# Optimization experiments

Measured on AMD Instinct MI355X. Metric: run time of the kernel, lower is better.

## Reference

```python
import jax, jax.numpy as jnp
import numpy as np

N = 8192
F_IN, F1, F2 = 11, 16, 32
HEADS = 3
D_CAT = 2 * F2          # 64, concat of interface + neighborhood branches
D_POOL = D_CAT * HEADS  # 192


def setup_inputs() -> dict:
    key = jax.random.key(0)
    ks = jax.random.split(key, 16)
    s = 0.1
    return {
        "x_int": jax.random.normal(ks[0], (N, F_IN), jnp.float32),
        "x_nh": jax.random.normal(ks[1], (N, F_IN), jnp.float32),
        # dense soft adjacencies, scaled ~1/N so aggregates stay O(1)
        "adj_int": jax.random.uniform(ks[2], (N, N), jnp.float32) / N,
        "adj_nh": jax.random.uniform(ks[3], (N, N), jnp.float32) / N,
        "W1_int": jax.random.normal(ks[4], (F_IN, F1), jnp.float32) * s,
        "b1_int": jnp.zeros((F1,), jnp.float32),
        "W1_nh": jax.random.normal(ks[5], (F_IN, F1), jnp.float32) * s,
        "b1_nh": jnp.zeros((F1,), jnp.float32),
        "W2_int": jax.random.normal(ks[6], (F1, F2), jnp.float32) * s,
        "b2_int": jnp.zeros((F2,), jnp.float32),
        "W2_nh": jax.random.normal(ks[7], (F1, F2), jnp.float32) * s,
        "b2_nh": jnp.zeros((F2,), jnp.float32),
        "W_att": jax.random.normal(ks[8], (D_CAT, HEADS), jnp.float32) * s,
        "W_dense": jax.random.normal(ks[9], (D_POOL, 1), jnp.float32) * s,
        "b_dense": jnp.zeros((1,), jnp.float32),
    }


def _dgcn(A, x, W, b):
    # diffusion graph conv: aggregate neighbors then linear + relu
    return jax.nn.relu(A @ (x @ W) + b)


def reference(x_int, x_nh, adj_int, adj_nh,
              W1_int, b1_int, W1_nh, b1_nh,
              W2_int, b2_int, W2_nh, b2_nh,
              W_att, W_dense, b_dense):
    # conv1 / conv2, two parallel graph branches
    h_int = _dgcn(adj_int, x_int, W1_int, b1_int)   # [N, 16]
    h_nh = _dgcn(adj_nh, x_nh, W1_nh, b1_nh)        # [N, 16]
    h_int = _dgcn(adj_int, h_int, W2_int, b2_int)   # [N, 32]
    h_nh = _dgcn(adj_nh, h_nh, W2_nh, b2_nh)        # [N, 32]
    h = jnp.concatenate([h_int, h_nh], axis=1)      # [N, 64]
    # multi-head tanh self-attention pooling over nodes
    scores = jnp.tanh(h @ W_att)                    # [N, heads]
    att = jax.nn.softmax(scores, axis=0)            # softmax over nodes
    pooled = jnp.einsum('nh,nd->hd', att, h).reshape(1, D_POOL)  # [1, 192]
    out = pooled @ W_dense + b_dense                # [1, 1]
    return jnp.squeeze(out, 1)                      # [1]
```

## Files before the change

kernel.cpp:

```cpp
#include <hip/hip_runtime.h>


constexpr int N = 8192;

__global__ void k_dense_in(const float* __restrict__ x0, const float* __restrict__ x1,
                           const float* __restrict__ W0, const float* __restrict__ W1,
                           float* __restrict__ o0, float* __restrict__ o1) {
    const int branch = blockIdx.y;
    const float* __restrict__ x = branch ? x1 : x0;
    const float* __restrict__ W = branch ? W1 : W0;
    float* __restrict__ o = branch ? o1 : o0;
    __shared__ float sW[11 * 16];
    if (threadIdx.x < 176) sW[threadIdx.x] = W[threadIdx.x];
    __syncthreads();
    const int n = blockIdx.x * blockDim.x + threadIdx.x;
    float xr[11];
#pragma unroll
    for (int j = 0; j < 11; ++j) xr[j] = x[n * 11 + j];
    float acc[16];
#pragma unroll
    for (int f = 0; f < 16; ++f) acc[f] = 0.f;
#pragma unroll
    for (int j = 0; j < 11; ++j)
#pragma unroll
        for (int f = 0; f < 16; ++f) acc[f] += xr[j] * sW[j * 16 + f];
#pragma unroll
    for (int f = 0; f < 16; ++f) o[f * N + n] = acc[f];
}

__global__ void k_dense_mid(const float* __restrict__ h0, const float* __restrict__ h1,
                            const float* __restrict__ W0, const float* __restrict__ W1,
                            float* __restrict__ o0, float* __restrict__ o1) {
    const int branch = blockIdx.y;
    const float* __restrict__ h = branch ? h1 : h0;
    const float* __restrict__ W = branch ? W1 : W0;
    float* __restrict__ o = branch ? o1 : o0;
    __shared__ float sW[16 * 32];
    for (int i = threadIdx.x; i < 512; i += blockDim.x) sW[i] = W[i];
    __syncthreads();
    const int n = blockIdx.x * blockDim.x + threadIdx.x;
    float hr[16];
#pragma unroll
    for (int q = 0; q < 4; ++q)
        *reinterpret_cast<float4*>(&hr[q * 4]) =
            *reinterpret_cast<const float4*>(&h[n * 16 + q * 4]);
    float acc[32];
#pragma unroll
    for (int f = 0; f < 32; ++f) acc[f] = 0.f;
#pragma unroll
    for (int j = 0; j < 16; ++j)
#pragma unroll
        for (int f = 0; f < 32; ++f) acc[f] += hr[j] * sW[j * 32 + f];
#pragma unroll
    for (int f = 0; f < 32; ++f) o[f * N + n] = acc[f];
}

template <int F>
__global__ __launch_bounds__(256, F == 16 ? 3 : 2) void k_spmm(
    const float* __restrict__ A0, const float* __restrict__ A1,
    const float* __restrict__ PT0, const float* __restrict__ PT1,
    const float* __restrict__ b0, const float* __restrict__ b1,
    float* __restrict__ o0, float* __restrict__ o1, int ostride) {
    constexpr int Fw = F / 4;
    constexpr int M = 8;
    constexpr int KT = 256;
    constexpr int NT = N / KT;
    constexpr int NV = M * Fw;
    const int branch = blockIdx.y;
    const float* __restrict__ A = branch ? A1 : A0;
    const float* __restrict__ PT = branch ? PT1 : PT0;
    const float* __restrict__ bias = branch ? b1 : b0;
    float* __restrict__ o = branch ? o1 : o0;

    const int lane = threadIdx.x & 63;
    const int wave = threadIdx.x >> 6;
    const int f0 = wave * Fw;
    const int r0 = blockIdx.x * M;
    const int phase = blockIdx.x & (NT - 1);

    const float* __restrict__ Abase = A + (size_t)r0 * N + 4 * lane;
    const float* __restrict__ Pbase = PT + (size_t)f0 * N + 4 * lane;

    float4 a[M], an[M], pt[Fw];
    float acc[M][Fw];
#pragma unroll
    for (int m = 0; m < M; ++m)
#pragma unroll
        for (int j = 0; j < Fw; ++j) acc[m][j] = 0.f;

    auto K0of = [&](int t) { return ((t + phase) & (NT - 1)) * KT; };
    auto loadA = [&](float4(&buf)[M], int K0) {
#pragma unroll
        for (int m = 0; m < M; ++m)
            buf[m] = *reinterpret_cast<const float4*>(Abase + (size_t)m * N + K0);
    };
    auto loadP = [&](int K0) {
#pragma unroll
        for (int j = 0; j < Fw; ++j)
            pt[j] = *reinterpret_cast<const float4*>(Pbase + (size_t)j * N + K0);
    };
    auto fmas = [&](float4(&buf)[M]) {
#pragma unroll
        for (int m = 0; m < M; ++m)
#pragma unroll
            for (int j = 0; j < Fw; ++j) {
                acc[m][j] += buf[m].x * pt[j].x;
                acc[m][j] += buf[m].y * pt[j].y;
                acc[m][j] += buf[m].z * pt[j].z;
                acc[m][j] += buf[m].w * pt[j].w;
            }
    };

    loadA(a, K0of(0));
    for (int t = 0; t < NT; t += 2) {
        loadP(K0of(t));
        loadA(an, K0of(t + 1));
        __builtin_amdgcn_s_barrier();
        fmas(a);
        loadP(K0of(t + 1));
        if (t + 2 < NT) loadA(a, K0of(t + 2));
        __builtin_amdgcn_s_barrier();
        fmas(an);
    }

    float v[NV];
#pragma unroll
    for (int i = 0; i < NV; ++i) v[i] = acc[i / Fw][i % Fw];
#pragma unroll
    for (int s = 0; (NV >> s) > 1; ++s) {
        const int bit = (lane >> s) & 1;
#pragma unroll
        for (int i = 0; i < (NV >> s); i += 2) {
            const float t0 = __shfl_xor(v[i], 1 << s);
            const float t1 = __shfl_xor(v[i + 1], 1 << s);
            v[i >> 1] = bit ? (v[i + 1] + t1) : (v[i] + t0);
        }
    }
    float r = v[0];
    if constexpr (NV == 32) r += __shfl_xor(r, 32);

    const int m = lane / Fw;
    const int j = lane % Fw;
    if (F == 32 || lane < 32) {
        const float val = fmaxf(r + bias[f0 + j], 0.f);
        o[(size_t)(r0 + m) * ostride + f0 + j] = val;
    }
}

__global__ void k_att_pool(const float* __restrict__ h, const float* __restrict__ Watt,
                           const float* __restrict__ Wd, float* __restrict__ partials) {
    __shared__ float sWa[64 * 3];
    __shared__ float sWd[192];
    for (int i = threadIdx.x; i < 192; i += blockDim.x) {
        sWa[i] = Watt[i];
        sWd[i] = Wd[i];
    }
    __syncthreads();
    const int n = blockIdx.x * blockDim.x + threadIdx.x;
    float hv[64];
#pragma unroll
    for (int q = 0; q < 16; ++q)
        *reinterpret_cast<float4*>(&hv[q * 4]) =
            *reinterpret_cast<const float4*>(&h[(size_t)n * 64 + q * 4]);
    float s0 = 0.f, s1 = 0.f, s2 = 0.f;
#pragma unroll
    for (int d = 0; d < 64; ++d) {
        s0 += hv[d] * sWa[d * 3 + 0];
        s1 += hv[d] * sWa[d * 3 + 1];
        s2 += hv[d] * sWa[d * 3 + 2];
    }
    float dot0 = 0.f, dot1 = 0.f, dot2 = 0.f;
#pragma unroll
    for (int d = 0; d < 64; ++d) {
        dot0 += hv[d] * sWd[0 * 64 + d];
        dot1 += hv[d] * sWd[1 * 64 + d];
        dot2 += hv[d] * sWd[2 * 64 + d];
    }
    const float e0 = expf(tanhf(s0));
    const float e1 = expf(tanhf(s1));
    const float e2 = expf(tanhf(s2));
    float vals[6] = {e0, e1, e2, e0 * dot0, e1 * dot1, e2 * dot2};
#pragma unroll
    for (int i = 0; i < 6; ++i) {
        float v = vals[i];
#pragma unroll
        for (int off = 1; off < 64; off <<= 1) v += __shfl_xor(v, off);
        vals[i] = v;
    }
    __shared__ float sred[4][6];
    const int wave = threadIdx.x >> 6, lane = threadIdx.x & 63;
    if (lane == 0) {
#pragma unroll
        for (int i = 0; i < 6; ++i) sred[wave][i] = vals[i];
    }
    __syncthreads();
    if (threadIdx.x == 0) {
#pragma unroll
        for (int i = 0; i < 6; ++i)
            partials[blockIdx.x * 6 + i] = sred[0][i] + sred[1][i] + sred[2][i] + sred[3][i];
    }
}

__global__ void k_att_final(const float* __restrict__ partials, const float* __restrict__ bd,
                            float* __restrict__ out) {
    if (threadIdx.x == 0) {
        float Z0 = 0.f, Z1 = 0.f, Z2 = 0.f, U0 = 0.f, U1 = 0.f, U2 = 0.f;
        for (int b = 0; b < 32; ++b) {
            Z0 += partials[b * 6 + 0];
            Z1 += partials[b * 6 + 1];
            Z2 += partials[b * 6 + 2];
            U0 += partials[b * 6 + 3];
            U1 += partials[b * 6 + 4];
            U2 += partials[b * 6 + 5];
        }
        out[0] = U0 / Z0 + U1 / Z1 + U2 / Z2 + bd[0];
    }
}

extern "C" void kernel_launch(void* const* d_in, const int* in_sizes, int n_in,
                              void* d_out, int out_size, void* d_ws, size_t ws_size,
                              hipStream_t stream) {
    const float* x_int   = (const float*)d_in[0];
    const float* x_nh    = (const float*)d_in[1];
    const float* adj_int = (const float*)d_in[2];
    const float* adj_nh  = (const float*)d_in[3];
    const float* W1_int  = (const float*)d_in[4];
    const float* b1_int  = (const float*)d_in[5];
    const float* W1_nh   = (const float*)d_in[6];
    const float* b1_nh   = (const float*)d_in[7];
    const float* W2_int  = (const float*)d_in[8];
    const float* b2_int  = (const float*)d_in[9];
    const float* W2_nh   = (const float*)d_in[10];
    const float* b2_nh   = (const float*)d_in[11];
    const float* W_att   = (const float*)d_in[12];
    const float* W_dense = (const float*)d_in[13];
    const float* b_dense = (const float*)d_in[14];

    float* ws = (float*)d_ws;
    float* P1T_0 = ws;
    float* P1T_1 = ws + 131072;
    float* H1_0  = ws + 262144;
    float* H1_1  = ws + 393216;
    float* P2T_0 = ws + 524288;
    float* P2T_1 = ws + 786432;
    float* hcat  = ws + 1048576;
    float* partials = ws + 1572864;
    float* out = (float*)d_out;

    k_dense_in<<<dim3(32, 2), 256, 0, stream>>>(x_int, x_nh, W1_int, W1_nh, P1T_0, P1T_1);
    k_spmm<16><<<dim3(1024, 2), 256, 0, stream>>>(adj_int, adj_nh, P1T_0, P1T_1,
                                                  b1_int, b1_nh, H1_0, H1_1, 16);
    k_dense_mid<<<dim3(32, 2), 256, 0, stream>>>(H1_0, H1_1, W2_int, W2_nh, P2T_0, P2T_1);
    k_spmm<32><<<dim3(1024, 2), 256, 0, stream>>>(adj_int, adj_nh, P2T_0, P2T_1,
                                                  b2_int, b2_nh, hcat, hcat + 32, 64);
    k_att_pool<<<32, 256, 0, stream>>>(hcat, W_att, W_dense, partials);
    k_att_final<<<1, 64, 0, stream>>>(partials, b_dense, out);
}
```

Before: 626.5 us.

## Split-K dense SpMM with LDS-staged P tiles and separate reduction kernel

Restructures the adjacency-times-features kernels into a split-K scheme. Each 512-thread block handles 128 rows and one K slice, stages the transposed P slice into shared memory in two feature halves, and streams A rows with double buffering. Partial sums go to a workspace and are combined by a new reduce kernel that adds bias and applies ReLU. The aim is to cut redundant global reads of P and raise reuse and occupancy in the memory-bound A stream. The cost is an extra partials write and read plus an additional kernel launch per layer.

After: 1.565 ms. 2.5x slower.

```diff
diff --git a/kernel.cpp b/kernel.cpp
--- a/kernel.cpp
+++ b/kernel.cpp
@@ -1,4 +1,5 @@
 #include <hip/hip_runtime.h>
+#include <type_traits>
 
 
 constexpr int N = 8192;
@@ -56,95 +57,151 @@
 }
 
 template <int F>
-__global__ __launch_bounds__(256, F == 16 ? 3 : 2) void k_spmm(
+__global__ __launch_bounds__(512, 2) void k_spmm(
     const float* __restrict__ A0, const float* __restrict__ A1,
     const float* __restrict__ PT0, const float* __restrict__ PT1,
-    const float* __restrict__ b0, const float* __restrict__ b1,
-    float* __restrict__ o0, float* __restrict__ o1, int ostride) {
-    constexpr int Fw = F / 4;
-    constexpr int M = 8;
-    constexpr int KT = 256;
-    constexpr int NT = N / KT;
-    constexpr int NV = M * Fw;
-    const int branch = blockIdx.y;
-    const float* __restrict__ A = branch ? A1 : A0;
-    const float* __restrict__ PT = branch ? PT1 : PT0;
-    const float* __restrict__ bias = branch ? b1 : b0;
-    float* __restrict__ o = branch ? o1 : o0;
-
-    const int lane = threadIdx.x & 63;
-    const int wave = threadIdx.x >> 6;
-    const int f0 = wave * Fw;
-    const int r0 = blockIdx.x * M;
-    const int phase = blockIdx.x & (NT - 1);
-
-    const float* __restrict__ Abase = A + (size_t)r0 * N + 4 * lane;
-    const float* __restrict__ Pbase = PT + (size_t)f0 * N + 4 * lane;
-
-    float4 a[M], an[M], pt[Fw];
-    float acc[M][Fw];
-#pragma unroll
-    for (int m = 0; m < M; ++m)
-#pragma unroll
-        for (int j = 0; j < Fw; ++j) acc[m][j] = 0.f;
-
-    auto K0of = [&](int t) { return ((t + phase) & (NT - 1)) * KT; };
-    auto loadA = [&](float4(&buf)[M], int K0) {
-#pragma unroll
-        for (int m = 0; m < M; ++m)
-            buf[m] = *reinterpret_cast<const float4*>(Abase + (size_t)m * N + K0);
+    float* __restrict__ part) {
+    constexpr int W = 32768 / F;
+    constexpr int NS = N / W;
+    constexpr int C = W / 256;
+    constexpr int G2 = F / 8;
+    constexpr int NG = 8;
+    constexpr int RPB = 128;
+
+    const int br = blockIdx.y;
+    const float* __restrict__ A = br ? A1 : A0;
+    const float* __restrict__ PT = br ? PT1 : PT0;
+    float* __restrict__ pb = part + (size_t)br * NS * N * F;
+
+    __shared__ float plds[16384];
+
+    const int tid = threadIdx.x;
+    const int lane = tid & 63;
+    const int wave = tid >> 6;
+    const int rb = blockIdx.x / NS, sl = blockIdx.x % NS;
+    const int K0 = sl * W;
+    const int wrow0 = rb * RPB + wave * (2 * NG);
+
+    const float* __restrict__ Ab = A + (size_t)wrow0 * N + K0 + 4 * lane;
+
+    auto stage = [&](int half) {
+        const float* __restrict__ Ps = PT + (size_t)half * (F / 2) * N + K0;
+        for (int idx = tid; idx < (F / 2) * W; idx += 512) {
+            const int kk = idx & (W - 1);
+            const int fl = idx / W;
+            plds[((kk & 3) * G2 + (fl >> 2)) * W + ((kk >> 2) << 2) + (fl & 3)] =
+                Ps[(size_t)fl * N + kk];
+        }
     };
-    auto loadP = [&](int K0) {
-#pragma unroll
-        for (int j = 0; j < Fw; ++j)
-            pt[j] = *reinterpret_cast<const float4*>(Pbase + (size_t)j * N + K0);
+
+    float acc[2][F];
+#pragma unroll
+    for (int rr = 0; rr < 2; ++rr)
+#pragma unroll
+        for (int f = 0; f < F; ++f) acc[rr][f] = 0.f;
+
+    float4 Abuf[2][C], Bbuf[2][C];
+
+    auto ld = [&](float4(&buf)[2][C], int g) {
+#pragma unroll
+        for (int rr = 0; rr < 2; ++rr)
+#pragma unroll
+            for (int c = 0; c < C; ++c)
+                buf[rr][c] = *reinterpret_cast<const float4*>(
+                    Ab + (size_t)(2 * g + rr) * N + c * 256);
     };
-    auto fmas = [&](float4(&buf)[M]) {
-#pragma unroll
-        for (int m = 0; m < M; ++m)
-#pragma unroll
-            for (int j = 0; j < Fw; ++j) {
-                acc[m][j] += buf[m].x * pt[j].x;
-                acc[m][j] += buf[m].y * pt[j].y;
-                acc[m][j] += buf[m].z * pt[j].z;
-                acc[m][j] += buf[m].w * pt[j].w;
+
+    auto cmp = [&](auto Hc, float4(&buf)[2][C]) {
+        constexpr int HALF = decltype(Hc)::value;
+#pragma unroll
+        for (int c = 0; c < C; ++c)
+#pragma unroll
+            for (int t = 0; t < 4; ++t)
+#pragma unroll
+                for (int g = 0; g < G2; ++g) {
+                    const float4 pv = *reinterpret_cast<const float4*>(
+                        &plds[(t * G2 + g) * W + (c * 64 + lane) * 4]);
+#pragma unroll
+                    for (int rr = 0; rr < 2; ++rr) {
+                        const float av = (t == 0)   ? buf[rr][c].x
+                                         : (t == 1) ? buf[rr][c].y
+                                         : (t == 2) ? buf[rr][c].z
+                                                    : buf[rr][c].w;
+                        acc[rr][HALF * (F / 2) + g * 4 + 0] += av * pv.x;
+                        acc[rr][HALF * (F / 2) + g * 4 + 1] += av * pv.y;
+                        acc[rr][HALF * (F / 2) + g * 4 + 2] += av * pv.z;
+                        acc[rr][HALF * (F / 2) + g * 4 + 3] += av * pv.w;
+                    }
+                }
+    };
+
+    auto redstore = [&](int g) {
+        constexpr int NV = 2 * F;
+        float v[NV];
+#pragma unroll
+        for (int i = 0; i < NV; ++i) v[i] = acc[i / F][i % F];
+#pragma unroll
+        for (int s = 0; (NV >> s) > 1; ++s) {
+            const int bit = (lane >> s) & 1;
+#pragma unroll
+            for (int i = 0; i < (NV >> s); i += 2) {
+                const float t0 = __shfl_xor(v[i], 1 << s);
+                const float t1 = __shfl_xor(v[i + 1], 1 << s);
+                v[i >> 1] = bit ? (v[i + 1] + t1) : (v[i] + t0);
             }
+        }
+        float r = v[0];
+        if constexpr (NV == 32) {
+            r += __shfl_xor(r, 32);
+            if (lane < 32)
+                pb[((size_t)sl * N + wrow0 + 2 * g + (lane >> 4)) * F + (lane & 15)] = r;
+        } else {
+            pb[((size_t)sl * N + wrow0 + 2 * g + (lane >> 5)) * F + (lane & 31)] = r;
+        }
+#pragma unroll
+        for (int rr = 0; rr < 2; ++rr)
+#pragma unroll
+            for (int f = 0; f < F; ++f) acc[rr][f] = 0.f;
     };
 
-    loadA(a, K0of(0));
-    for (int t = 0; t < NT; t += 2) {
-        loadP(K0of(t));
-        loadA(an, K0of(t + 1));
-        __builtin_amdgcn_s_barrier();
-        fmas(a);
-        loadP(K0of(t + 1));
-        if (t + 2 < NT) loadA(a, K0of(t + 2));
-        __builtin_amdgcn_s_barrier();
-        fmas(an);
-    }
-
-    float v[NV];
-#pragma unroll
-    for (int i = 0; i < NV; ++i) v[i] = acc[i / Fw][i % Fw];
-#pragma unroll
-    for (int s = 0; (NV >> s) > 1; ++s) {
-        const int bit = (lane >> s) & 1;
-#pragma unroll
-        for (int i = 0; i < (NV >> s); i += 2) {
-            const float t0 = __shfl_xor(v[i], 1 << s);
-            const float t1 = __shfl_xor(v[i + 1], 1 << s);
-            v[i >> 1] = bit ? (v[i + 1] + t1) : (v[i] + t0);
-        }
-    }
-    float r = v[0];
-    if constexpr (NV == 32) r += __shfl_xor(r, 32);
-
-    const int m = lane / Fw;
-    const int j = lane % Fw;
-    if (F == 32 || lane < 32) {
-        const float val = fmaxf(r + bias[f0 + j], 0.f);
-        o[(size_t)(r0 + m) * ostride + f0 + j] = val;
-    }
+    using IC0 = std::integral_constant<int, 0>;
+    using IC1 = std::integral_constant<int, 1>;
+
+    stage(0);
+    ld(Abuf, 0);
+    __syncthreads();
+    for (int gp = 0; gp < NG; gp += 2) {
+        ld(Bbuf, gp + 1);
+        cmp(IC0{}, Abuf);
+        __syncthreads();
+        stage(1);
+        __syncthreads();
+        cmp(IC1{}, Abuf);
+        redstore(gp);
+        if (gp + 2 < NG) ld(Abuf, gp + 2);
+        cmp(IC1{}, Bbuf);
+        __syncthreads();
+        stage(0);
+        __syncthreads();
+        cmp(IC0{}, Bbuf);
+        redstore(gp + 1);
+    }
+}
+
+template <int F, int NS>
+__global__ void k_reduce(const float* __restrict__ part,
+                         const float* __restrict__ bias0, const float* __restrict__ bias1,
+                         float* __restrict__ o0, float* __restrict__ o1, int ostride) {
+    const int br = blockIdx.y;
+    const float* __restrict__ pb = part + (size_t)br * NS * N * F;
+    const float* __restrict__ bias = br ? bias1 : bias0;
+    float* __restrict__ o = br ? o1 : o0;
+    const int i = blockIdx.x * 256 + threadIdx.x;
+    const int r = i / F, f = i % F;
+    float s = bias[f];
+#pragma unroll
+    for (int sl = 0; sl < NS; ++sl) s += pb[(size_t)sl * N * F + i];
+    o[(size_t)r * ostride + f] = fmaxf(s, 0.f);
 }
 
 __global__ void k_att_pool(const float* __restrict__ h, const float* __restrict__ Watt,
@@ -244,15 +301,16 @@
     float* P2T_0 = ws + 524288;
     float* P2T_1 = ws + 786432;
     float* hcat  = ws + 1048576;
-    float* partials = ws + 1572864;
+    float* attp  = ws + 1572864;
+    float* part  = ws + 1573120;
     float* out = (float*)d_out;
 
     k_dense_in<<<dim3(32, 2), 256, 0, stream>>>(x_int, x_nh, W1_int, W1_nh, P1T_0, P1T_1);
-    k_spmm<16><<<dim3(1024, 2), 256, 0, stream>>>(adj_int, adj_nh, P1T_0, P1T_1,
-                                                  b1_int, b1_nh, H1_0, H1_1, 16);
+    k_spmm<16><<<dim3(256, 2), 512, 0, stream>>>(adj_int, adj_nh, P1T_0, P1T_1, part);
+    k_reduce<16, 4><<<dim3(512, 2), 256, 0, stream>>>(part, b1_int, b1_nh, H1_0, H1_1, 16);
     k_dense_mid<<<dim3(32, 2), 256, 0, stream>>>(H1_0, H1_1, W2_int, W2_nh, P2T_0, P2T_1);
-    k_spmm<32><<<dim3(1024, 2), 256, 0, stream>>>(adj_int, adj_nh, P2T_0, P2T_1,
-                                                  b2_int, b2_nh, hcat, hcat + 32, 64);
-    k_att_pool<<<32, 256, 0, stream>>>(hcat, W_att, W_dense, partials);
-    k_att_final<<<1, 64, 0, stream>>>(partials, b_dense, out);
-}
+    k_spmm<32><<<dim3(512, 2), 512, 0, stream>>>(adj_int, adj_nh, P2T_0, P2T_1, part);
+    k_reduce<32, 8><<<dim3(1024, 2), 256, 0, stream>>>(part, b2_int, b2_nh, hcat, hcat + 32, 64);
+    k_att_pool<<<32, 256, 0, stream>>>(hcat, W_att, W_dense, attp);
+    k_att_final<<<1, 64, 0, stream>>>(attp, b_dense, out);
+}
```
